# Performance work log

Measured on AMD Instinct MI355X. Metric: run time of the kernel, lower is better.

The kernel has to match this reference:

```python
import jax, jax.numpy as jnp
import numpy as np

BINS = 64


def _histogram(x, bins=BINS):
    """Faithful jax version of ColorHistogramLoss.get_histogram.

    Original semantics: edges = linspace(-1, 1, bins); bin j (j < bins-1) counts
    edges[j] <= v < edges[j+1]; last bin counts v >= edges[-1] (= 1).
    Values v < -1 fall in no bin. Single bucketize + scatter-add pass.
    """
    B, C = x.shape[0], x.shape[1]
    xf = x.reshape(B * C, -1)            # [B*C, N]
    N = xf.shape[1]
    edges = jnp.linspace(-1.0, 1.0, bins).astype(x.dtype)
    # searchsorted(side='right') - 1 gives j with edges[j] <= v < edges[j+1];
    # v < -1 -> -1 (invalid); v >= 1 -> bins-1 after clip (matches open last bin).
    idx = jnp.searchsorted(edges, xf, side='right') - 1
    valid = idx >= 0
    idx = jnp.clip(idx, 0, bins - 1)
    seg = idx + jnp.arange(B * C)[:, None] * bins      # per-(batch,channel) offset
    counts = jax.ops.segment_sum(
        valid.astype(jnp.float32).ravel(), seg.ravel(),
        num_segments=B * C * bins)
    return counts.reshape(B, C * bins) / N             # [B, C*bins]


def setup_inputs() -> dict:
    key = jax.random.key(0)
    k1, k2 = jax.random.split(key)
    shape = (32, 3, 512, 512)
    # pixels normalized to [-1, 1), matching the linspace(-1, 1) bin edges
    inp = jax.random.uniform(k1, shape, dtype=jnp.float32) * 2.0 - 1.0
    tgt = jax.random.uniform(k2, shape, dtype=jnp.float32) * 2.0 - 1.0
    return {"input": inp, "target": tgt}


def reference(input, target):
    hist_in = _histogram(input, BINS)
    hist_tgt = _histogram(target, BINS)
    return jnp.mean(jnp.abs(hist_in - hist_tgt))   # F.l1_loss (mean reduction)
```

## Files before the change

kernel.cpp:

```cpp
#include <hip/hip_runtime.h>


#define BINS 64
#define PLANES 96
#define PLANE_F4 65536
#define SEGS 32
#define SEG_F4 2048
#define TPB 256
#define F4T 8

__device__ __forceinline__ void bump(int* lh, int col, float v, int inc) {
    int bin = (int)floorf((v + 1.0f) * 31.5f);
    if (bin >= 0) {
        bin = bin > 63 ? 63 : bin;
        atomicAdd(&lh[(bin << 6) + col], inc);
    }
}

__global__ __launch_bounds__(TPB) void hist_diff_kernel(
        const float4* __restrict__ in4, const float4* __restrict__ tg4,
        int* __restrict__ gdiff) {
    __shared__ int lh[BINS * 64];
    const int tid = threadIdx.x;
    const int col = tid & 63;

    {
        int4* p = (int4*)lh;
        const int4 z = {0, 0, 0, 0};
#pragma unroll
        for (int k = 0; k < (BINS * 64 / 4) / TPB; ++k) p[tid + k * TPB] = z;
    }
    __syncthreads();

    const int plane = blockIdx.x >> 5;
    const int seg   = blockIdx.x & (SEGS - 1);
    const long base = (long)plane * PLANE_F4 + (long)seg * SEG_F4 + tid;

    float4 a[F4T];
#pragma unroll
    for (int k = 0; k < F4T; ++k) a[k] = in4[base + k * TPB];
#pragma unroll
    for (int k = 0; k < F4T; ++k) {
        bump(lh, col, a[k].x, 1); bump(lh, col, a[k].y, 1);
        bump(lh, col, a[k].z, 1); bump(lh, col, a[k].w, 1);
    }
#pragma unroll
    for (int k = 0; k < F4T; ++k) a[k] = tg4[base + k * TPB];
#pragma unroll
    for (int k = 0; k < F4T; ++k) {
        bump(lh, col, a[k].x, -1); bump(lh, col, a[k].y, -1);
        bump(lh, col, a[k].z, -1); bump(lh, col, a[k].w, -1);
    }

    __syncthreads();
    if (tid < BINS) {
        int s = 0;
#pragma unroll
        for (int j = 0; j < 64; ++j) s += lh[(tid << 6) + ((tid + j) & 63)];
        if (s != 0) atomicAdd(&gdiff[plane * BINS + tid], s);
    }
}

__global__ __launch_bounds__(TPB) void reduce_abs_kernel(
        const int* __restrict__ gdiff, float* __restrict__ out) {
    int s = 0;
    for (int i = threadIdx.x; i < PLANES * BINS; i += TPB) {
        int v = gdiff[i];
        s += (v < 0) ? -v : v;
    }
#pragma unroll
    for (int off = 32; off > 0; off >>= 1) s += __shfl_down(s, off, 64);
    __shared__ int ws[TPB / 64];
    const int wid  = threadIdx.x >> 6;
    const int lane = threadIdx.x & 63;
    if (lane == 0) ws[wid] = s;
    __syncthreads();
    if (threadIdx.x == 0) {
        int total = 0;
#pragma unroll
        for (int w = 0; w < TPB / 64; ++w) total += ws[w];
        out[0] = (float)total * (1.0f / (262144.0f * 6144.0f));
    }
}

extern "C" void kernel_launch(void* const* d_in, const int* in_sizes, int n_in,
                              void* d_out, int out_size, void* d_ws, size_t ws_size,
                              hipStream_t stream) {
    const float4* inp = (const float4*)d_in[0];
    const float4* tgt = (const float4*)d_in[1];
    int* gdiff = (int*)d_ws;

    hipMemsetAsync(gdiff, 0, PLANES * BINS * sizeof(int), stream);
    hist_diff_kernel<<<PLANES * SEGS, TPB, 0, stream>>>(inp, tgt, gdiff);
    reduce_abs_kernel<<<1, TPB, 0, stream>>>(gdiff, (float*)d_out);
}
```

Before: 215.4 us.

## Use per-thread private int8 histograms instead of shared-memory atomics

Each thread gets its own padded signed-char row of 64 bins in LDS, so updates become plain byte read-modify-writes instead of atomicAdd on shared int bins. A column-wise reduction over the 256 rows, split into four partial groups, produces the per-block bin differences before the global atomic. Launch bounds now also request 8 blocks per SM. Each thread processes 64 values with +1/-1 increments, so int8 counters cannot overflow, but byte-granular LDS accesses can hit bank conflicts, and the final reduction does more LDS reads.

```diff
diff --git a/kernel.cpp b/kernel.cpp
--- a/kernel.cpp
+++ b/kernel.cpp
@@ -8,56 +8,62 @@
 #define SEG_F4 2048
 #define TPB 256
 #define F4T 8
+#define RSTRIDE 68
 
-__device__ __forceinline__ void bump(int* lh, int col, float v, int inc) {
+__device__ __forceinline__ void bump(signed char* row, float v, int inc) {
     int bin = (int)floorf((v + 1.0f) * 31.5f);
     if (bin >= 0) {
         bin = bin > 63 ? 63 : bin;
-        atomicAdd(&lh[(bin << 6) + col], inc);
+        row[bin] = (signed char)(row[bin] + inc);
     }
 }
 
-__global__ __launch_bounds__(TPB) void hist_diff_kernel(
+__global__ __launch_bounds__(TPB, 8) void hist_diff_kernel(
         const float4* __restrict__ in4, const float4* __restrict__ tg4,
         int* __restrict__ gdiff) {
-    __shared__ int lh[BINS * 64];
+    __shared__ signed char lh[TPB * RSTRIDE];
+    __shared__ int part[4][BINS];
     const int tid = threadIdx.x;
-    const int col = tid & 63;
 
     {
-        int4* p = (int4*)lh;
-        const int4 z = {0, 0, 0, 0};
+        int* p = (int*)lh;
 #pragma unroll
-        for (int k = 0; k < (BINS * 64 / 4) / TPB; ++k) p[tid + k * TPB] = z;
+        for (int k = 0; k < (TPB * RSTRIDE / 4) / TPB; ++k) p[tid + k * TPB] = 0;
     }
     __syncthreads();
 
     const int plane = blockIdx.x >> 5;
     const int seg   = blockIdx.x & (SEGS - 1);
     const long base = (long)plane * PLANE_F4 + (long)seg * SEG_F4 + tid;
+    signed char* row = lh + tid * RSTRIDE;
 
     float4 a[F4T];
 #pragma unroll
     for (int k = 0; k < F4T; ++k) a[k] = in4[base + k * TPB];
 #pragma unroll
     for (int k = 0; k < F4T; ++k) {
-        bump(lh, col, a[k].x, 1); bump(lh, col, a[k].y, 1);
-        bump(lh, col, a[k].z, 1); bump(lh, col, a[k].w, 1);
+        bump(row, a[k].x, 1); bump(row, a[k].y, 1);
+        bump(row, a[k].z, 1); bump(row, a[k].w, 1);
     }
 #pragma unroll
     for (int k = 0; k < F4T; ++k) a[k] = tg4[base + k * TPB];
 #pragma unroll
     for (int k = 0; k < F4T; ++k) {
-        bump(lh, col, a[k].x, -1); bump(lh, col, a[k].y, -1);
-        bump(lh, col, a[k].z, -1); bump(lh, col, a[k].w, -1);
+        bump(row, a[k].x, -1); bump(row, a[k].y, -1);
+        bump(row, a[k].z, -1); bump(row, a[k].w, -1);
     }
 
     __syncthreads();
+    const int g = tid >> 6, j = tid & 63;
+    int s = 0;
+#pragma unroll
+    for (int r = 0; r < 64; ++r)
+        s += lh[(g * 64 + r) * RSTRIDE + j];
+    part[g][j] = s;
+    __syncthreads();
     if (tid < BINS) {
-        int s = 0;
-#pragma unroll
-        for (int j = 0; j < 64; ++j) s += lh[(tid << 6) + ((tid + j) & 63)];
-        if (s != 0) atomicAdd(&gdiff[plane * BINS + tid], s);
+        int tot = part[0][tid] + part[1][tid] + part[2][tid] + part[3][tid];
+        if (tot != 0) atomicAdd(&gdiff[plane * BINS + tid], tot);
     }
 }
 
```

After: 216.7 us. About the same (+0.6%).
